# Kernel tuning notes

Measured on AMD Instinct MI355X. Metric: run time of the kernel, lower is better.

## Reference

```python
import jax, jax.numpy as jnp
import numpy as np
import math

N, L, S, H, E, D = 2, 2048, 2048, 16, 64, 64

def setup_inputs() -> dict:
    key = jax.random.key(0)
    kq, kk, kv = jax.random.split(key, 3)
    return {
        "queries": jax.random.normal(kq, (N, L, H, E), dtype=jnp.float32),
        "keys": jax.random.normal(kk, (N, S, H, E), dtype=jnp.float32),
        "values": jax.random.normal(kv, (N, S, H, D), dtype=jnp.float32),
        "attn_mask": jnp.zeros((L, S), dtype=jnp.float32),  # additive mask
    }

def reference(queries, keys, values, attn_mask):
    e = queries.shape[-1]
    softmax_temp = 1.0 / math.sqrt(e)  # self.softmax_temp is None -> 1/sqrt(E)
    # (N,L,H,E) x (N,S,H,E) -> (N,H,L,S)
    qk = jnp.einsum('nlhe,nshe->nhls', queries, keys)
    qk = qk + attn_mask  # additive mask broadcast over (N,H)
    att = jax.nn.softmax(softmax_temp * qk, axis=-1)
    # dropout rate 0.0 (eval) -> identity
    v = jnp.einsum('nhls,nshd->nlhd', att, values)
    return v
```

## Files before the change

kernel.cpp:

```cpp
#include <hip/hip_runtime.h>
#include <hip/hip_bf16.h>


typedef short bf16x8 __attribute__((ext_vector_type(8)));
typedef short short4v __attribute__((ext_vector_type(4)));
typedef unsigned uint2v __attribute__((ext_vector_type(2)));
typedef float f32x4 __attribute__((ext_vector_type(4)));

constexpr int Nb = 2, Lq = 2048, Sk = 2048, Hh = 16, Ee = 64, Dd = 64;
constexpr int BM = 128;
constexpr int BN = 64;
constexpr int NT = Sk / BN;
constexpr int KVB = Nb * Hh * NT * 16 * 64 / 256;
constexpr float SCALE_LOG2E = 0.125f * 1.4426950408889634f;

__device__ __forceinline__ short f2bf(float f) {
  union { float f; unsigned u; } v; v.f = f;
  unsigned r = (v.u + 0x7fffu + ((v.u >> 16) & 1u)) >> 16;
  return (short)r;
}

__device__ __forceinline__ unsigned pack_bf16x2(float a, float b) {
  union { __hip_bfloat162 h; unsigned u; } v;
  float2 f; f.x = a; f.y = b;
  v.h = __float22bfloat162_rn(f);
  return v.u;
}

__device__ __forceinline__ void async_copy16(const void* g, void* l) {
  __builtin_amdgcn_global_load_lds(
      (const __attribute__((address_space(1))) unsigned int*)g,
      (__attribute__((address_space(3))) unsigned int*)l, 16, 0, 0);
}

__global__ __launch_bounds__(256) void prep_all(const float* __restrict__ K,
                                                const float* __restrict__ V,
                                                const float* __restrict__ M,
                                                short* __restrict__ KVf,
                                                short* __restrict__ Mg) {
  if (blockIdx.x < KVB) {
    int gid = blockIdx.x * 256 + threadIdx.x;
    int l = gid & 63;
    int chunkid = gid >> 6;
    int ch = chunkid & 15;
    int t  = (chunkid >> 4) & 31;
    int nh = chunkid >> 9;
    int n = nh >> 4, h = nh & 15;
    int c = l & 15, quad = l >> 4;
    bf16x8 o;
    if (ch < 8) {
      int sb = ch >> 1, kc = ch & 1;
      int s = t * 64 + sb * 16 + c;
      int e0 = kc * 32 + quad * 8;
      const float* p = K + (((size_t)n * Sk + s) * Hh + h) * Ee + e0;
      float4 x = *(const float4*)(p);
      float4 y = *(const float4*)(p + 4);
      o[0] = f2bf(x.x); o[1] = f2bf(x.y); o[2] = f2bf(x.z); o[3] = f2bf(x.w);
      o[4] = f2bf(y.x); o[5] = f2bf(y.y); o[6] = f2bf(y.z); o[7] = f2bf(y.w);
    } else {
      int db = (ch - 8) >> 1, kc = (ch - 8) & 1;
      int d = db * 16 + c;
      int s0 = t * 64 + kc * 32 + quad * 8;
      const float* p = V + (((size_t)n * Sk + s0) * Hh + h) * Dd + d;
#pragma unroll
      for (int j = 0; j < 8; ++j) o[j] = f2bf(p[(size_t)j * Hh * Dd]);
    }
    *(bf16x8*)(KVf + (size_t)gid * 8) = o;
  } else {
    int u = (blockIdx.x - KVB) * 256 + threadIdx.x;
    int grow = u & 511;
    int l = u >> 9;
    int t = grow >> 4, g = grow & 15;
    int qt = l >> 7, lloc = l & 127;
    float4 mv = *(const float4*)(M + (size_t)l * Sk + grow * 4);
    short4v o;
    o[0] = f2bf(mv.x * SCALE_LOG2E); o[1] = f2bf(mv.y * SCALE_LOG2E);
    o[2] = f2bf(mv.z * SCALE_LOG2E); o[3] = f2bf(mv.w * SCALE_LOG2E);
    size_t dst = ((((size_t)qt * NT + t) * 128 + lloc) << 6) + ((g ^ (lloc & 15)) << 2);
    *(short4v*)(Mg + dst) = o;
  }
}

__global__ __launch_bounds__(256) void attn_fwd(
    const float* __restrict__ Q, const short* __restrict__ KVf,
    const short* __restrict__ Mg, float* __restrict__ Out)
{
  __shared__ short KV[2][8192];
  __shared__ short Ms[2][8192];
  __shared__ short Ps[4][2048];

  const int tid  = threadIdx.x;
  const int lane = tid & 63;
  const int w    = tid >> 6;
  const int quad = lane >> 4;
  const int c    = lane & 15;

  const int id   = blockIdx.x;
  const int slot = id >> 3;
  const int qt   = slot & 15;
  const int nh   = (id & 7) * 4 + (slot >> 4);
  const int n    = nh >> 4;
  const int h    = nh & 15;

  const int row0 = qt * BM + w * 32;

  bf16x8 qfrag[2][2];
#pragma unroll
  for (int cb = 0; cb < 2; ++cb) {
    const float* qp = Q + (((size_t)n * Lq + (row0 + cb * 16 + c)) * Hh + h) * Ee;
#pragma unroll
    for (int kc = 0; kc < 2; ++kc) {
      const float* p = qp + kc * 32 + quad * 8;
      float4 x = *(const float4*)(p);
      float4 y = *(const float4*)(p + 4);
      bf16x8 f;
      f[0] = f2bf(x.x * SCALE_LOG2E); f[1] = f2bf(x.y * SCALE_LOG2E);
      f[2] = f2bf(x.z * SCALE_LOG2E); f[3] = f2bf(x.w * SCALE_LOG2E);
      f[4] = f2bf(y.x * SCALE_LOG2E); f[5] = f2bf(y.y * SCALE_LOG2E);
      f[6] = f2bf(y.z * SCALE_LOG2E); f[7] = f2bf(y.w * SCALE_LOG2E);
      qfrag[cb][kc] = f;
    }
  }

  f32x4 o[2][4];
#pragma unroll
  for (int cb = 0; cb < 2; ++cb)
#pragma unroll
    for (int db = 0; db < 4; ++db) { o[cb][db][0] = 0.f; o[cb][db][1] = 0.f; o[cb][db][2] = 0.f; o[cb][db][3] = 0.f; }
  float rs[2] = {0.f, 0.f};

  const short* kvt = KVf + (size_t)nh * NT * 8192;
  const short* mqt = Mg  + (size_t)qt * NT * 8192;

#pragma unroll
  for (int i = 0; i < 4; ++i) {
    int ch = w * 4 + i;
    async_copy16(kvt + ch * 512 + lane * 8, &KV[0][ch * 512 + lane * 8]);
    async_copy16(mqt + ch * 512 + lane * 8, &Ms[0][ch * 512 + lane * 8]);
  }
  __syncthreads();

  for (int t = 0; t < NT; ++t) {
    const int buf = t & 1;

    if (t + 1 < NT) {
      const short* gk = kvt + (size_t)(t + 1) * 8192;
      const short* gm = mqt + (size_t)(t + 1) * 8192;
#pragma unroll
      for (int i = 0; i < 4; ++i) {
        int ch = w * 4 + i;
        async_copy16(gk + ch * 512 + lane * 8, &KV[buf ^ 1][ch * 512 + lane * 8]);
        async_copy16(gm + ch * 512 + lane * 8, &Ms[buf ^ 1][ch * 512 + lane * 8]);
      }
    }

    const short* kb = &KV[buf][0];

    f32x4 sacc[2][4];
#pragma unroll
    for (int cb = 0; cb < 2; ++cb)
#pragma unroll
      for (int sb = 0; sb < 4; ++sb) {
        int row = w * 32 + cb * 16 + c;
        int gp = ((4 * sb + quad) ^ c) * 4;
        uint2v mv = *(const uint2v*)&Ms[buf][row * 64 + gp];
        sacc[cb][sb][0] = __uint_as_float(mv.x << 16);
        sacc[cb][sb][1] = __uint_as_float(mv.x & 0xffff0000u);
        sacc[cb][sb][2] = __uint_as_float(mv.y << 16);
        sacc[cb][sb][3] = __uint_as_float(mv.y & 0xffff0000u);
      }

#pragma unroll
    for (int kc = 0; kc < 2; ++kc) {
#pragma unroll
      for (int sb = 0; sb < 4; ++sb) {
        bf16x8 kfrag = *(const bf16x8*)&kb[(sb * 2 + kc) * 512 + lane * 8];
#pragma unroll
        for (int cb = 0; cb < 2; ++cb)
          sacc[cb][sb] = __builtin_amdgcn_mfma_f32_16x16x32_bf16(kfrag, qfrag[cb][kc], sacc[cb][sb], 0, 0, 0);
      }
    }

#pragma unroll
    for (int cb = 0; cb < 2; ++cb)
#pragma unroll
      for (int sb = 0; sb < 4; ++sb) {
        float p0 = __builtin_amdgcn_exp2f(sacc[cb][sb][0]);
        float p1 = __builtin_amdgcn_exp2f(sacc[cb][sb][1]);
        float p2 = __builtin_amdgcn_exp2f(sacc[cb][sb][2]);
        float p3 = __builtin_amdgcn_exp2f(sacc[cb][sb][3]);
        rs[cb] += (p0 + p1) + (p2 + p3);
        uint2v pv;
        pv.x = pack_bf16x2(p0, p1);
        pv.y = pack_bf16x2(p2, p3);
        int gp = ((4 * sb + quad) ^ c) * 4;
        *(uint2v*)&Ps[w][(cb * 16 + c) * 64 + gp] = pv;
      }

#pragma unroll
    for (int kc = 0; kc < 2; ++kc) {
      bf16x8 pfrag[2];
#pragma unroll
      for (int cb = 0; cb < 2; ++cb) {
        int G0 = 8 * kc + 2 * quad;
        int ga = (G0 ^ c) * 4, gb = ((G0 + 1) ^ c) * 4;
        union { uint2v u[2]; bf16x8 f; } uu;
        uu.u[0] = *(const uint2v*)&Ps[w][(cb * 16 + c) * 64 + ga];
        uu.u[1] = *(const uint2v*)&Ps[w][(cb * 16 + c) * 64 + gb];
        pfrag[cb] = uu.f;
      }
#pragma unroll
      for (int db = 0; db < 4; ++db) {
        bf16x8 vfrag = *(const bf16x8*)&kb[(8 + db * 2 + kc) * 512 + lane * 8];
#pragma unroll
        for (int cb = 0; cb < 2; ++cb)
          o[cb][db] = __builtin_amdgcn_mfma_f32_16x16x32_bf16(vfrag, pfrag[cb], o[cb][db], 0, 0, 0);
      }
    }

    __syncthreads();
  }

#pragma unroll
  for (int cb = 0; cb < 2; ++cb) {
    float v = rs[cb];
    v += __shfl_xor(v, 16, 64);
    v += __shfl_xor(v, 32, 64);
    float inv = 1.0f / v;
    float* op = Out + (((size_t)n * Lq + (row0 + cb * 16 + c)) * Hh + h) * Dd + quad * 4;
#pragma unroll
    for (int db = 0; db < 4; ++db) {
      float4 ov;
      ov.x = o[cb][db][0] * inv; ov.y = o[cb][db][1] * inv;
      ov.z = o[cb][db][2] * inv; ov.w = o[cb][db][3] * inv;
      *(float4*)(op + db * 16) = ov;
    }
  }
}

extern "C" void kernel_launch(void* const* d_in, const int* in_sizes, int n_in,
                              void* d_out, int out_size, void* d_ws, size_t ws_size,
                              hipStream_t stream) {
  const float* Q   = (const float*)d_in[0];
  const float* K   = (const float*)d_in[1];
  const float* V   = (const float*)d_in[2];
  const float* Msk = (const float*)d_in[3];
  float* Out = (float*)d_out;

  short* KVf = (short*)d_ws;
  short* Mg  = KVf + (size_t)Nb * Hh * NT * 8192;

  prep_all<<<dim3(KVB + 4096), dim3(256), 0, stream>>>(K, V, Msk, KVf, Mg);

  attn_fwd<<<dim3((Lq / BM) * Nb * Hh), dim3(256), 0, stream>>>(Q, KVf, Mg, Out);
}
```

Measured before the change: 177.8 us.

## Halve query tile and stream mask per-lane from global into registers

Shrinks the query tile from 128 to 64 rows, so each wave handles 16 rows and the grid doubles. The mask is repacked so each lane can load its MFMA fragment straight from global memory into registers, prefetched one tile ahead. This drops the shared-memory mask buffer and lowers LDS use, with launch bounds asking for 4 blocks per CU for occupancy. In exchange, K/V tiles are reused across half as many query rows, so LDS and global traffic for K/V per output row doubles.

```diff
diff --git a/kernel.cpp b/kernel.cpp
--- a/kernel.cpp
+++ b/kernel.cpp
@@ -8,7 +8,7 @@
 typedef float f32x4 __attribute__((ext_vector_type(4)));
 
 constexpr int Nb = 2, Lq = 2048, Sk = 2048, Hh = 16, Ee = 64, Dd = 64;
-constexpr int BM = 128;
+constexpr int BM = 64;
 constexpr int BN = 64;
 constexpr int NT = Sk / BN;
 constexpr int KVB = Nb * Hh * NT * 16 * 64 / 256;
@@ -68,26 +68,26 @@
     *(bf16x8*)(KVf + (size_t)gid * 8) = o;
   } else {
     int u = (blockIdx.x - KVB) * 256 + threadIdx.x;
-    int grow = u & 511;
-    int l = u >> 9;
-    int t = grow >> 4, g = grow & 15;
-    int qt = l >> 7, lloc = l & 127;
-    float4 mv = *(const float4*)(M + (size_t)l * Sk + grow * 4);
+    int colg = u & 511;
+    int row  = u >> 9;
+    int qt = row >> 6, wv = (row >> 4) & 3, c = row & 15;
+    int t = colg >> 4, sb = (colg >> 2) & 3, quad = colg & 3;
+    int lane = quad * 16 + c;
+    float4 mv = *(const float4*)(M + (size_t)row * Sk + colg * 4);
     short4v o;
     o[0] = f2bf(mv.x * SCALE_LOG2E); o[1] = f2bf(mv.y * SCALE_LOG2E);
     o[2] = f2bf(mv.z * SCALE_LOG2E); o[3] = f2bf(mv.w * SCALE_LOG2E);
-    size_t dst = ((((size_t)qt * NT + t) * 128 + lloc) << 6) + ((g ^ (lloc & 15)) << 2);
-    *(short4v*)(Mg + dst) = o;
-  }
-}
-
-__global__ __launch_bounds__(256) void attn_fwd(
+    size_t gran = ((((size_t)(qt * 4 + wv) * 32 + t) * 4 + sb) * 64) + lane;
+    *(short4v*)(Mg + gran * 4) = o;
+  }
+}
+
+__global__ __launch_bounds__(256, 4) void attn_fwd(
     const float* __restrict__ Q, const short* __restrict__ KVf,
     const short* __restrict__ Mg, float* __restrict__ Out)
 {
   __shared__ short KV[2][8192];
-  __shared__ short Ms[2][8192];
-  __shared__ short Ps[4][2048];
+  __shared__ short Ps[4][1024];
 
   const int tid  = threadIdx.x;
   const int lane = tid & 63;
@@ -97,17 +97,17 @@
 
   const int id   = blockIdx.x;
   const int slot = id >> 3;
-  const int qt   = slot & 15;
-  const int nh   = (id & 7) * 4 + (slot >> 4);
+  const int qt   = slot & 31;
+  const int nh   = (id & 7) * 4 + (slot >> 5);
   const int n    = nh >> 4;
   const int h    = nh & 15;
 
-  const int row0 = qt * BM + w * 32;
-
-  bf16x8 qfrag[2][2];
-#pragma unroll
-  for (int cb = 0; cb < 2; ++cb) {
-    const float* qp = Q + (((size_t)n * Lq + (row0 + cb * 16 + c)) * Hh + h) * Ee;
+  const int row0 = qt * BM + w * 16;
+  const int qrow = row0 + c;
+
+  bf16x8 qfrag[2];
+  {
+    const float* qp = Q + (((size_t)n * Lq + qrow) * Hh + h) * Ee;
 #pragma unroll
     for (int kc = 0; kc < 2; ++kc) {
       const float* p = qp + kc * 32 + quad * 8;
@@ -118,26 +118,26 @@
       f[2] = f2bf(x.z * SCALE_LOG2E); f[3] = f2bf(x.w * SCALE_LOG2E);
       f[4] = f2bf(y.x * SCALE_LOG2E); f[5] = f2bf(y.y * SCALE_LOG2E);
       f[6] = f2bf(y.z * SCALE_LOG2E); f[7] = f2bf(y.w * SCALE_LOG2E);
-      qfrag[cb][kc] = f;
-    }
-  }
-
-  f32x4 o[2][4];
-#pragma unroll
-  for (int cb = 0; cb < 2; ++cb)
-#pragma unroll
-    for (int db = 0; db < 4; ++db) { o[cb][db][0] = 0.f; o[cb][db][1] = 0.f; o[cb][db][2] = 0.f; o[cb][db][3] = 0.f; }
-  float rs[2] = {0.f, 0.f};
+      qfrag[kc] = f;
+    }
+  }
+
+  f32x4 o[4];
+#pragma unroll
+  for (int db = 0; db < 4; ++db) { o[db][0] = 0.f; o[db][1] = 0.f; o[db][2] = 0.f; o[db][3] = 0.f; }
+  float rs = 0.f;
 
   const short* kvt = KVf + (size_t)nh * NT * 8192;
-  const short* mqt = Mg  + (size_t)qt * NT * 8192;
+  const short* mp = Mg + ((size_t)(qt * 4 + w) * 32) * 1024 + lane * 4;
 
 #pragma unroll
   for (int i = 0; i < 4; ++i) {
     int ch = w * 4 + i;
     async_copy16(kvt + ch * 512 + lane * 8, &KV[0][ch * 512 + lane * 8]);
-    async_copy16(mqt + ch * 512 + lane * 8, &Ms[0][ch * 512 + lane * 8]);
-  }
+  }
+  uint2v mcur[4], mnxt[4];
+#pragma unroll
+  for (int sb = 0; sb < 4; ++sb) mcur[sb] = *(const uint2v*)(mp + sb * 256);
   __syncthreads();
 
   for (int t = 0; t < NT; ++t) {
@@ -145,96 +145,80 @@
 
     if (t + 1 < NT) {
       const short* gk = kvt + (size_t)(t + 1) * 8192;
-      const short* gm = mqt + (size_t)(t + 1) * 8192;
 #pragma unroll
       for (int i = 0; i < 4; ++i) {
         int ch = w * 4 + i;
         async_copy16(gk + ch * 512 + lane * 8, &KV[buf ^ 1][ch * 512 + lane * 8]);
-        async_copy16(gm + ch * 512 + lane * 8, &Ms[buf ^ 1][ch * 512 + lane * 8]);
       }
+      const short* gm = mp + (size_t)(t + 1) * 1024;
+#pragma unroll
+      for (int sb = 0; sb < 4; ++sb) mnxt[sb] = *(const uint2v*)(gm + sb * 256);
     }
 
     const short* kb = &KV[buf][0];
 
-    f32x4 sacc[2][4];
-#pragma unroll
-    for (int cb = 0; cb < 2; ++cb)
-#pragma unroll
-      for (int sb = 0; sb < 4; ++sb) {
-        int row = w * 32 + cb * 16 + c;
-        int gp = ((4 * sb + quad) ^ c) * 4;
-        uint2v mv = *(const uint2v*)&Ms[buf][row * 64 + gp];
-        sacc[cb][sb][0] = __uint_as_float(mv.x << 16);
-        sacc[cb][sb][1] = __uint_as_float(mv.x & 0xffff0000u);
-        sacc[cb][sb][2] = __uint_as_float(mv.y << 16);
-        sacc[cb][sb][3] = __uint_as_float(mv.y & 0xffff0000u);
-      }
+    f32x4 sacc[4];
+#pragma unroll
+    for (int sb = 0; sb < 4; ++sb) {
+      sacc[sb][0] = __uint_as_float(mcur[sb].x << 16);
+      sacc[sb][1] = __uint_as_float(mcur[sb].x & 0xffff0000u);
+      sacc[sb][2] = __uint_as_float(mcur[sb].y << 16);
+      sacc[sb][3] = __uint_as_float(mcur[sb].y & 0xffff0000u);
+    }
 
 #pragma unroll
     for (int kc = 0; kc < 2; ++kc) {
 #pragma unroll
       for (int sb = 0; sb < 4; ++sb) {
         bf16x8 kfrag = *(const bf16x8*)&kb[(sb * 2 + kc) * 512 + lane * 8];
-#pragma unroll
-        for (int cb = 0; cb < 2; ++cb)
-          sacc[cb][sb] = __builtin_amdgcn_mfma_f32_16x16x32_bf16(kfrag, qfrag[cb][kc], sacc[cb][sb], 0, 0, 0);
+        sacc[sb] = __builtin_amdgcn_mfma_f32_16x16x32_bf16(kfrag, qfrag[kc], sacc[sb], 0, 0, 0);
       }
     }
 
 #pragma unroll
-    for (int cb = 0; cb < 2; ++cb)
-#pragma unroll
-      for (int sb = 0; sb < 4; ++sb) {
-        float p0 = __builtin_amdgcn_exp2f(sacc[cb][sb][0]);
-        float p1 = __builtin_amdgcn_exp2f(sacc[cb][sb][1]);
-        float p2 = __builtin_amdgcn_exp2f(sacc[cb][sb][2]);
-        float p3 = __builtin_amdgcn_exp2f(sacc[cb][sb][3]);
-        rs[cb] += (p0 + p1) + (p2 + p3);
-        uint2v pv;
-        pv.x = pack_bf16x2(p0, p1);
-        pv.y = pack_bf16x2(p2, p3);
-        int gp = ((4 * sb + quad) ^ c) * 4;
-        *(uint2v*)&Ps[w][(cb * 16 + c) * 64 + gp] = pv;
-      }
+    for (int sb = 0; sb < 4; ++sb) {
+      float p0 = __builtin_amdgcn_exp2f(sacc[sb][0]);
+      float p1 = __builtin_amdgcn_exp2f(sacc[sb][1]);
+      float p2 = __builtin_amdgcn_exp2f(sacc[sb][2]);
+      float p3 = __builtin_amdgcn_exp2f(sacc[sb][3]);
+      rs += (p0 + p1) + (p2 + p3);
+      uint2v pv;
+      pv.x = pack_bf16x2(p0, p1);
+      pv.y = pack_bf16x2(p2, p3);
+      int gp = ((4 * sb + quad) ^ c) * 4;
+      *(uint2v*)&Ps[w][c * 64 + gp] = pv;
+    }
 
 #pragma unroll
     for (int kc = 0; kc < 2; ++kc) {
-      bf16x8 pfrag[2];
-#pragma unroll
-      for (int cb = 0; cb < 2; ++cb) {
-        int G0 = 8 * kc + 2 * quad;
-        int ga = (G0 ^ c) * 4, gb = ((G0 + 1) ^ c) * 4;
-        union { uint2v u[2]; bf16x8 f; } uu;
-        uu.u[0] = *(const uint2v*)&Ps[w][(cb * 16 + c) * 64 + ga];
-        uu.u[1] = *(const uint2v*)&Ps[w][(cb * 16 + c) * 64 + gb];
-        pfrag[cb] = uu.f;
-      }
+      int G0 = 8 * kc + 2 * quad;
+      int ga = (G0 ^ c) * 4, gb = ((G0 + 1) ^ c) * 4;
+      union { uint2v u[2]; bf16x8 f; } uu;
+      uu.u[0] = *(const uint2v*)&Ps[w][c * 64 + ga];
+      uu.u[1] = *(const uint2v*)&Ps[w][c * 64 + gb];
+      bf16x8 pfrag = uu.f;
 #pragma unroll
       for (int db = 0; db < 4; ++db) {
         bf16x8 vfrag = *(const bf16x8*)&kb[(8 + db * 2 + kc) * 512 + lane * 8];
-#pragma unroll
-        for (int cb = 0; cb < 2; ++cb)
-          o[cb][db] = __builtin_amdgcn_mfma_f32_16x16x32_bf16(vfrag, pfrag[cb], o[cb][db], 0, 0, 0);
+        o[db] = __builtin_amdgcn_mfma_f32_16x16x32_bf16(vfrag, pfrag, o[db], 0, 0, 0);
       }
     }
 
     __syncthreads();
-  }
-
-#pragma unroll
-  for (int cb = 0; cb < 2; ++cb) {
-    float v = rs[cb];
-    v += __shfl_xor(v, 16, 64);
-    v += __shfl_xor(v, 32, 64);
-    float inv = 1.0f / v;
-    float* op = Out + (((size_t)n * Lq + (row0 + cb * 16 + c)) * Hh + h) * Dd + quad * 4;
-#pragma unroll
-    for (int db = 0; db < 4; ++db) {
-      float4 ov;
-      ov.x = o[cb][db][0] * inv; ov.y = o[cb][db][1] * inv;
-      ov.z = o[cb][db][2] * inv; ov.w = o[cb][db][3] * inv;
-      *(float4*)(op + db * 16) = ov;
-    }
+#pragma unroll
+    for (int sb = 0; sb < 4; ++sb) mcur[sb] = mnxt[sb];
+  }
+
+  rs += __shfl_xor(rs, 16, 64);
+  rs += __shfl_xor(rs, 32, 64);
+  float inv = 1.0f / rs;
+  float* op = Out + (((size_t)n * Lq + qrow) * Hh + h) * Dd + quad * 4;
+#pragma unroll
+  for (int db = 0; db < 4; ++db) {
+    float4 ov;
+    ov.x = o[db][0] * inv; ov.y = o[db][1] * inv;
+    ov.z = o[db][2] * inv; ov.w = o[db][3] * inv;
+    *(float4*)(op + db * 16) = ov;
   }
 }
 
```

Result: faster. 167.6 us (-5.7%).

## Split KV sequence across two blocks with combine pass, load mask directly to registers

Applied to the files above, without the earlier changes.

Splits the key sequence into two halves processed by separate blocks (split-K flash attention), writing unnormalized partial outputs and row sums, then adds a combine kernel that sums partials and normalizes. The mask is re-laid out so each lane reads its values directly from global memory into registers, dropping the mask LDS buffer, and the mask add moves into the exp step. P staging in LDS is halved by processing one column block at a time, and launch bounds request 4 blocks per CU. The changes aim to double the grid for better CU occupancy and cut LDS use, at the cost of an extra kernel launch and extra global traffic for partial outputs.

```diff
diff --git a/kernel.cpp b/kernel.cpp
--- a/kernel.cpp
+++ b/kernel.cpp
@@ -26,6 +26,9 @@
   v.h = __float22bfloat162_rn(f);
   return v.u;
 }
+
+__device__ __forceinline__ float bf_lo(unsigned u) { return __uint_as_float(u << 16); }
+__device__ __forceinline__ float bf_hi(unsigned u) { return __uint_as_float(u & 0xffff0000u); }
 
 __device__ __forceinline__ void async_copy16(const void* g, void* l) {
   __builtin_amdgcn_global_load_lds(
@@ -68,26 +71,28 @@
     *(bf16x8*)(KVf + (size_t)gid * 8) = o;
   } else {
     int u = (blockIdx.x - KVB) * 256 + threadIdx.x;
-    int grow = u & 511;
-    int l = u >> 9;
-    int t = grow >> 4, g = grow & 15;
-    int qt = l >> 7, lloc = l & 127;
-    float4 mv = *(const float4*)(M + (size_t)l * Sk + grow * 4);
+    int colg = u & 511;
+    int row  = u >> 9;
+    int qt = row >> 7, wv = (row >> 5) & 3, cb = (row >> 4) & 1, cc = row & 15;
+    int t = colg >> 4, sb = (colg >> 2) & 3, quad = colg & 3;
+    int lane = quad * 16 + cc;
+    float4 mv = *(const float4*)(M + (size_t)row * Sk + colg * 4);
     short4v o;
     o[0] = f2bf(mv.x * SCALE_LOG2E); o[1] = f2bf(mv.y * SCALE_LOG2E);
     o[2] = f2bf(mv.z * SCALE_LOG2E); o[3] = f2bf(mv.w * SCALE_LOG2E);
-    size_t dst = ((((size_t)qt * NT + t) * 128 + lloc) << 6) + ((g ^ (lloc & 15)) << 2);
-    *(short4v*)(Mg + dst) = o;
-  }
-}
-
-__global__ __launch_bounds__(256) void attn_fwd(
+    size_t gran = ((((size_t)((qt * 4 + wv) * 2 + cb) * 32 + t) * 4 + sb) * 64) + lane;
+    *(short4v*)(Mg + gran * 4) = o;
+  }
+}
+
+template <int NS>
+__global__ __launch_bounds__(256, 4) void attn_fwd(
     const float* __restrict__ Q, const short* __restrict__ KVf,
-    const short* __restrict__ Mg, float* __restrict__ Out)
+    const short* __restrict__ Mg, float* __restrict__ P0,
+    float* __restrict__ P1, float* __restrict__ rsW)
 {
   __shared__ short KV[2][8192];
-  __shared__ short Ms[2][8192];
-  __shared__ short Ps[4][2048];
+  __shared__ short Ps[4][1024];
 
   const int tid  = threadIdx.x;
   const int lane = tid & 63;
@@ -97,12 +102,14 @@
 
   const int id   = blockIdx.x;
   const int slot = id >> 3;
-  const int qt   = slot & 15;
-  const int nh   = (id & 7) * 4 + (slot >> 4);
+  const int nh   = (id & 7) * 4 + (slot & 3);
+  const int qt   = (slot >> 2) & 15;
+  const int sp   = (NS == 2) ? (slot >> 6) : 0;
   const int n    = nh >> 4;
   const int h    = nh & 15;
 
   const int row0 = qt * BM + w * 32;
+  const int t0 = sp * (NT / NS), tc = NT / NS;
 
   bf16x8 qfrag[2][2];
 #pragma unroll
@@ -130,27 +137,32 @@
   float rs[2] = {0.f, 0.f};
 
   const short* kvt = KVf + (size_t)nh * NT * 8192;
-  const short* mqt = Mg  + (size_t)qt * NT * 8192;
+  const short* mbase = Mg + (size_t)((qt * 4 + w) * 2) * 32768 + lane * 4;
 
 #pragma unroll
   for (int i = 0; i < 4; ++i) {
     int ch = w * 4 + i;
-    async_copy16(kvt + ch * 512 + lane * 8, &KV[0][ch * 512 + lane * 8]);
-    async_copy16(mqt + ch * 512 + lane * 8, &Ms[0][ch * 512 + lane * 8]);
+    async_copy16(kvt + ((size_t)t0 * 8192) + ch * 512 + lane * 8, &KV[0][ch * 512 + lane * 8]);
   }
   __syncthreads();
 
-  for (int t = 0; t < NT; ++t) {
-    const int buf = t & 1;
-
-    if (t + 1 < NT) {
+  for (int tt = 0; tt < tc; ++tt) {
+    const int t = t0 + tt;
+    const int buf = tt & 1;
+
+    uint2v mv[2][4];
+#pragma unroll
+    for (int cb = 0; cb < 2; ++cb)
+#pragma unroll
+      for (int sb = 0; sb < 4; ++sb)
+        mv[cb][sb] = *(const uint2v*)(mbase + ((size_t)cb * 32 + t) * 1024 + sb * 256);
+
+    if (tt + 1 < tc) {
       const short* gk = kvt + (size_t)(t + 1) * 8192;
-      const short* gm = mqt + (size_t)(t + 1) * 8192;
 #pragma unroll
       for (int i = 0; i < 4; ++i) {
         int ch = w * 4 + i;
         async_copy16(gk + ch * 512 + lane * 8, &KV[buf ^ 1][ch * 512 + lane * 8]);
-        async_copy16(gm + ch * 512 + lane * 8, &Ms[buf ^ 1][ch * 512 + lane * 8]);
       }
     }
 
@@ -160,16 +172,7 @@
 #pragma unroll
     for (int cb = 0; cb < 2; ++cb)
 #pragma unroll
-      for (int sb = 0; sb < 4; ++sb) {
-        int row = w * 32 + cb * 16 + c;
-        int gp = ((4 * sb + quad) ^ c) * 4;
-        uint2v mv = *(const uint2v*)&Ms[buf][row * 64 + gp];
-        sacc[cb][sb][0] = __uint_as_float(mv.x << 16);
-        sacc[cb][sb][1] = __uint_as_float(mv.x & 0xffff0000u);
-        sacc[cb][sb][2] = __uint_as_float(mv.y << 16);
-        sacc[cb][sb][3] = __uint_as_float(mv.y & 0xffff0000u);
-      }
-
+      for (int sb = 0; sb < 4; ++sb) { sacc[cb][sb][0] = 0.f; sacc[cb][sb][1] = 0.f; sacc[cb][sb][2] = 0.f; sacc[cb][sb][3] = 0.f; }
 #pragma unroll
     for (int kc = 0; kc < 2; ++kc) {
 #pragma unroll
@@ -181,61 +184,86 @@
       }
     }
 
-#pragma unroll
-    for (int cb = 0; cb < 2; ++cb)
+    bf16x8 pfrag[2][2];
+#pragma unroll
+    for (int cb = 0; cb < 2; ++cb) {
 #pragma unroll
       for (int sb = 0; sb < 4; ++sb) {
-        float p0 = __builtin_amdgcn_exp2f(sacc[cb][sb][0]);
-        float p1 = __builtin_amdgcn_exp2f(sacc[cb][sb][1]);
-        float p2 = __builtin_amdgcn_exp2f(sacc[cb][sb][2]);
-        float p3 = __builtin_amdgcn_exp2f(sacc[cb][sb][3]);
+        float p0 = __builtin_amdgcn_exp2f(sacc[cb][sb][0] + bf_lo(mv[cb][sb].x));
+        float p1 = __builtin_amdgcn_exp2f(sacc[cb][sb][1] + bf_hi(mv[cb][sb].x));
+        float p2 = __builtin_amdgcn_exp2f(sacc[cb][sb][2] + bf_lo(mv[cb][sb].y));
+        float p3 = __builtin_amdgcn_exp2f(sacc[cb][sb][3] + bf_hi(mv[cb][sb].y));
         rs[cb] += (p0 + p1) + (p2 + p3);
         uint2v pv;
         pv.x = pack_bf16x2(p0, p1);
         pv.y = pack_bf16x2(p2, p3);
         int gp = ((4 * sb + quad) ^ c) * 4;
-        *(uint2v*)&Ps[w][(cb * 16 + c) * 64 + gp] = pv;
-      }
-
-#pragma unroll
-    for (int kc = 0; kc < 2; ++kc) {
-      bf16x8 pfrag[2];
-#pragma unroll
-      for (int cb = 0; cb < 2; ++cb) {
+        *(uint2v*)&Ps[w][c * 64 + gp] = pv;
+      }
+#pragma unroll
+      for (int kc = 0; kc < 2; ++kc) {
         int G0 = 8 * kc + 2 * quad;
         int ga = (G0 ^ c) * 4, gb = ((G0 + 1) ^ c) * 4;
         union { uint2v u[2]; bf16x8 f; } uu;
-        uu.u[0] = *(const uint2v*)&Ps[w][(cb * 16 + c) * 64 + ga];
-        uu.u[1] = *(const uint2v*)&Ps[w][(cb * 16 + c) * 64 + gb];
-        pfrag[cb] = uu.f;
-      }
+        uu.u[0] = *(const uint2v*)&Ps[w][c * 64 + ga];
+        uu.u[1] = *(const uint2v*)&Ps[w][c * 64 + gb];
+        pfrag[cb][kc] = uu.f;
+      }
+    }
+
+#pragma unroll
+    for (int kc = 0; kc < 2; ++kc) {
 #pragma unroll
       for (int db = 0; db < 4; ++db) {
         bf16x8 vfrag = *(const bf16x8*)&kb[(8 + db * 2 + kc) * 512 + lane * 8];
 #pragma unroll
         for (int cb = 0; cb < 2; ++cb)
-          o[cb][db] = __builtin_amdgcn_mfma_f32_16x16x32_bf16(vfrag, pfrag[cb], o[cb][db], 0, 0, 0);
+          o[cb][db] = __builtin_amdgcn_mfma_f32_16x16x32_bf16(vfrag, pfrag[cb][kc], o[cb][db], 0, 0, 0);
       }
     }
 
     __syncthreads();
   }
 
+  float* P = (sp == 0) ? P0 : P1;
 #pragma unroll
   for (int cb = 0; cb < 2; ++cb) {
     float v = rs[cb];
     v += __shfl_xor(v, 16, 64);
     v += __shfl_xor(v, 32, 64);
-    float inv = 1.0f / v;
-    float* op = Out + (((size_t)n * Lq + (row0 + cb * 16 + c)) * Hh + h) * Dd + quad * 4;
+    const int qrow = row0 + cb * 16 + c;
+    if (quad == 0) rsW[(size_t)sp * 65536 + nh * 2048 + qrow] = v;
+    float* op = P + (((size_t)n * Lq + qrow) * Hh + h) * Dd + quad * 4;
 #pragma unroll
     for (int db = 0; db < 4; ++db) {
       float4 ov;
-      ov.x = o[cb][db][0] * inv; ov.y = o[cb][db][1] * inv;
-      ov.z = o[cb][db][2] * inv; ov.w = o[cb][db][3] * inv;
+      ov.x = o[cb][db][0]; ov.y = o[cb][db][1];
+      ov.z = o[cb][db][2]; ov.w = o[cb][db][3];
       *(float4*)(op + db * 16) = ov;
     }
   }
+}
+
+template <int NS>
+__global__ __launch_bounds__(256) void combine(float* __restrict__ Out,
+                                               const float* __restrict__ P1,
+                                               const float* __restrict__ rsW) {
+  int gid = blockIdx.x * 256 + threadIdx.x;
+  size_t i4 = (size_t)gid * 4;
+  int hh = (int)((i4 >> 6) & 15);
+  int l  = (int)((i4 >> 10) & 2047);
+  int nn = (int)(i4 >> 21);
+  int nh = nn * 16 + hh;
+  float rs = rsW[nh * 2048 + l];
+  float4 v = *(const float4*)(Out + i4);
+  if (NS == 2) {
+    rs += rsW[65536 + (size_t)nh * 2048 + l];
+    float4 b = *(const float4*)(P1 + i4);
+    v.x += b.x; v.y += b.y; v.z += b.z; v.w += b.w;
+  }
+  float inv = 1.0f / rs;
+  v.x *= inv; v.y *= inv; v.z *= inv; v.w *= inv;
+  *(float4*)(Out + i4) = v;
 }
 
 extern "C" void kernel_launch(void* const* d_in, const int* in_sizes, int n_in,
@@ -248,9 +276,20 @@
   float* Out = (float*)d_out;
 
   short* KVf = (short*)d_ws;
-  short* Mg  = KVf + (size_t)Nb * Hh * NT * 8192;
+  short* Mg  = KVf + (size_t)8388608;
+  float* rsW = (float*)(Mg + (size_t)4194304);
+  float* P1  = rsW + 131072;
+
+  const size_t need2 = 16777216u + 8388608u + 524288u + 16777216u;
+  const bool split = ws_size >= need2;
 
   prep_all<<<dim3(KVB + 4096), dim3(256), 0, stream>>>(K, V, Msk, KVf, Mg);
 
-  attn_fwd<<<dim3((Lq / BM) * Nb * Hh), dim3(256), 0, stream>>>(Q, KVf, Mg, Out);
-}
+  if (split) {
+    attn_fwd<2><<<dim3(1024), dim3(256), 0, stream>>>(Q, KVf, Mg, Out, P1, rsW);
+    combine<2><<<dim3(4096), dim3(256), 0, stream>>>(Out, P1, rsW);
+  } else {
+    attn_fwd<1><<<dim3(512), dim3(256), 0, stream>>>(Q, KVf, Mg, Out, P1, rsW);
+    combine<1><<<dim3(4096), dim3(256), 0, stream>>>(Out, P1, rsW);
+  }
+}
```

Result: faster. 171.0 us (-3.8%).
